# Optimization experiments

Hardware: AMD Instinct MI355X
Metric: run time of the kernel (lower is better)

Reference implementation:

```python
import jax, jax.numpy as jnp
import numpy as np

N = 100000      # nodes
E = 3200000     # edges
F_IN = 256      # in_channels
H = 64          # hidden_channels
C = 2           # out_channels
G = 128         # graphs in batch


def setup_inputs() -> dict:
    key = jax.random.key(0)
    ks = jax.random.split(key, 10)
    x = jax.random.normal(ks[0], (N, F_IN), jnp.float32)
    edge_index = jax.random.randint(ks[1], (2, E), 0, N, dtype=jnp.int64)
    batch = jnp.sort(jax.random.randint(ks[2], (N,), 0, G, dtype=jnp.int64))
    s = 0.05
    W1 = jax.random.normal(ks[3], (F_IN, H), jnp.float32) * s
    b1 = jnp.zeros((H,), jnp.float32)
    W2 = jax.random.normal(ks[4], (H, H), jnp.float32) * s
    b2 = jnp.zeros((H,), jnp.float32)
    fc_W = jax.random.normal(ks[5], (H, C), jnp.float32) * s
    fc_b = jnp.zeros((C,), jnp.float32)
    return {"x": x, "edge_index": edge_index, "batch": batch,
            "W1": W1, "b1": b1, "W2": W2, "b2": b2,
            "fc_W": fc_W, "fc_b": fc_b}


def _gcn_layer(h, src, dst, norm, W, b, n_nodes):
    # PyG GCNConv: linear transform first, then normalized aggregate, then bias
    h = h @ W                                   # [N, H]
    msg = h[src] * norm[:, None]                # [E+N, H] gather + scale
    out = jax.ops.segment_sum(msg, dst, num_segments=n_nodes)
    return out + b


def reference(x, edge_index, batch, W1, b1, W2, b2, fc_W, fc_b):
    n_nodes = x.shape[0]
    # add self loops (GCNConv default)
    loop = jnp.arange(n_nodes, dtype=edge_index.dtype)
    src = jnp.concatenate([edge_index[0], loop])
    dst = jnp.concatenate([edge_index[1], loop])
    # symmetric normalization D^{-1/2} (A+I) D^{-1/2}
    deg = jax.ops.segment_sum(jnp.ones_like(src, dtype=x.dtype), dst,
                              num_segments=n_nodes)
    deg_isqrt = jnp.where(deg > 0, jax.lax.rsqrt(deg), 0.0)
    norm = deg_isqrt[src] * deg_isqrt[dst]

    h = jax.nn.relu(_gcn_layer(x, src, dst, norm, W1, b1, n_nodes))
    h = jax.nn.relu(_gcn_layer(h, src, dst, norm, W2, b2, n_nodes))

    # global mean pool over graphs
    n_graphs = G
    sums = jax.ops.segment_sum(h, batch, num_segments=n_graphs)
    cnts = jax.ops.segment_sum(jnp.ones((n_nodes,), h.dtype), batch,
                               num_segments=n_graphs)
    pooled = sums / jnp.clip(cnts, 1.0)[:, None]  # [G, H]
    return pooled @ fc_W + fc_b                   # [G, C]
```

## Files before the change

kernel.cpp:

```cpp
#include <hip/hip_runtime.h>
#include <hip/hip_bf16.h>


#define F_IN 256
#define HDIM 64
#define BR_SHIFT 7
#define BRANGE 128
#define BCAP 4608
#define CHUNK 8192
#define NBK 788

typedef short short8 __attribute__((ext_vector_type(8)));
typedef short short4v __attribute__((ext_vector_type(4)));
typedef float float4v __attribute__((ext_vector_type(4)));
typedef _Float16 half_t;

__device__ __forceinline__ unsigned bf16_rn(float f) {
  unsigned u = __builtin_bit_cast(unsigned, f);
  return (u + 0x7FFFu + ((u >> 16) & 1u)) >> 16;
}
__device__ __forceinline__ float bf16_to_f32(unsigned h) {
  return __builtin_bit_cast(float, h << 16);
}

__global__ __launch_bounds__(256) void bin_kernel(
    const int* __restrict__ src, const int* __restrict__ dst,
    int* __restrict__ gcur, int* __restrict__ entries, int E, int nb) {
  __shared__ int out32[CHUNK];
  __shared__ int pref[NBK + 1];
  __shared__ int cur[NBK];
  __shared__ int gbase[NBK];
  __shared__ int sscan[256];
  const int tid = threadIdx.x;
  for (int i = tid; i < nb; i += 256) cur[i] = 0;
  __syncthreads();
  long e0 = (long)blockIdx.x * CHUNK;
  int cnt = (int)min((long)CHUNK, (long)E - e0);
  for (int i = tid; i < cnt; i += 256)
    atomicAdd(&cur[dst[e0 + i] >> BR_SHIFT], 1);
  __syncthreads();
  int b0 = tid * 4;
  int h[4];
  int s = 0;
#pragma unroll
  for (int i = 0; i < 4; ++i) {
    h[i] = (b0 + i < nb) ? cur[b0 + i] : 0;
    s += h[i];
  }
  int x = s;
  sscan[tid] = x;
  __syncthreads();
  for (int off = 1; off < 256; off <<= 1) {
    int t = (tid >= off) ? sscan[tid - off] : 0;
    __syncthreads();
    sscan[tid] += t;
    __syncthreads();
  }
  int run = sscan[tid] - x;
#pragma unroll
  for (int i = 0; i < 4; ++i) {
    if (b0 + i < nb) {
      pref[b0 + i] = run;
      cur[b0 + i] = run;
      if (h[i] > 0) gbase[b0 + i] = atomicAdd(&gcur[b0 + i], h[i]);
      run += h[i];
    }
  }
  if (tid == 0) pref[nb] = cnt;
  __syncthreads();
  for (int i = tid; i < cnt; i += 256) {
    int d = dst[e0 + i];
    int sv = src[e0 + i];
    int b = d >> BR_SHIFT;
    int r = atomicAdd(&cur[b], 1);
    out32[r] = ((d & (BRANGE - 1)) << 17) | sv;
  }
  __syncthreads();
  for (int j = tid; j < cnt; j += 256) {
    int lo = 0, hi = nb - 1;
    while (lo < hi) {
      int mid = (lo + hi + 1) >> 1;
      if (pref[mid] <= j) lo = mid; else hi = mid - 1;
    }
    int b = lo;
    int slot = gbase[b] + (j - pref[b]);
    if (slot < BCAP) entries[(size_t)b * BCAP + slot] = out32[j];
  }
}

__global__ __launch_bounds__(256) void bucket_scan_kernel(
    const int* __restrict__ gcur, int* __restrict__ bbase,
    int* __restrict__ rowptr, int nb, int N, int E) {
  __shared__ int sscan[256];
  const int tid = threadIdx.x;
  int b0 = tid * 4;
  int h[4];
  int s = 0;
#pragma unroll
  for (int i = 0; i < 4; ++i) {
    h[i] = (b0 + i < nb) ? min(gcur[b0 + i], BCAP) : 0;
    s += h[i];
  }
  int x = s;
  sscan[tid] = x;
  __syncthreads();
  for (int off = 1; off < 256; off <<= 1) {
    int t = (tid >= off) ? sscan[tid - off] : 0;
    __syncthreads();
    sscan[tid] += t;
    __syncthreads();
  }
  int run = sscan[tid] - x;
#pragma unroll
  for (int i = 0; i < 4; ++i) {
    if (b0 + i < nb) {
      bbase[b0 + i] = run;
      run += h[i];
    }
  }
  if (tid == 0) rowptr[N] = E;
}

__global__ __launch_bounds__(256) void csr_build_kernel(
    const int* __restrict__ entries, const int* __restrict__ gcur,
    const int* __restrict__ bbase, int* __restrict__ rowptr,
    float* __restrict__ dnorm, int* __restrict__ csr, int N) {
  __shared__ int lbuf[BCAP];
  __shared__ int lcnt[BRANGE];
  __shared__ int lpref[BRANGE];
  __shared__ int lcur[BRANGE];
  const int b = blockIdx.x, tid = threadIdx.x;
  const int v0 = b * BRANGE;
  const int nloc = min(BRANGE, N - v0);
  if (tid < BRANGE) lcnt[tid] = 0;
  __syncthreads();
  const int cnt = min(gcur[b], BCAP);
  const int base = bbase[b];
  const int* ep = entries + (size_t)b * BCAP;
  for (int i = tid; i < cnt; i += 256) atomicAdd(&lcnt[ep[i] >> 17], 1);
  __syncthreads();
  if (tid < BRANGE) lpref[tid] = lcnt[tid];
  __syncthreads();
  for (int off = 1; off < BRANGE; off <<= 1) {
    int t = 0;
    if (tid < BRANGE && tid >= off) t = lpref[tid - off];
    __syncthreads();
    if (tid < BRANGE) lpref[tid] += t;
    __syncthreads();
  }
  if (tid < BRANGE) {
    int excl = lpref[tid] - lcnt[tid];
    lcur[tid] = excl;
    if (tid < nloc) {
      rowptr[v0 + tid] = base + excl;
      dnorm[v0 + tid] = rsqrtf((float)lcnt[tid] + 1.0f);
    }
  }
  __syncthreads();
  for (int i = tid; i < cnt; i += 256) {
    int e = ep[i];
    int dl = e >> 17;
    int pos = atomicAdd(&lcur[dl], 1);
    if (pos < BCAP) lbuf[pos] = e & 0x1FFFF;
  }
  __syncthreads();
  int* outp = csr + base;
  for (int i = tid; i < cnt; i += 256) outp[i] = lbuf[i];
}

template <int K>
__global__ __launch_bounds__(256) void wfrag_kernel(
    const float* __restrict__ W, short* __restrict__ whi,
    short* __restrict__ wlo) {
  constexpr int KS = K / 32;
  int slot = blockIdx.x * 256 + threadIdx.x;
  if (slot >= 4 * KS * 64 * 8) return;
  int j = slot & 7;
  int lane = (slot >> 3) & 63;
  int fk = slot >> 9;
  int ks = fk % KS;
  int ct = fk / KS;
  int k = ks * 32 + (lane >> 4) * 8 + j;
  int n = ct * 16 + (lane & 15);
  float w = W[k * 64 + n];
  unsigned h = bf16_rn(w);
  unsigned l = bf16_rn(w - bf16_to_f32(h));
  whi[slot] = (short)h;
  wlo[slot] = (short)l;
}

template <int K, typename OT>
__global__ __launch_bounds__(512) void mfma_gemm_kernel(
    const float* __restrict__ X, const short* __restrict__ whi,
    const short* __restrict__ wlo, const float* __restrict__ dnorm,
    OT* __restrict__ out, int N) {
  constexpr int KS = K / 32;
  constexpr int P = K + 8;
  __shared__ __align__(16) short Ahi[64 * P];
  __shared__ __align__(16) short Alo[64 * P];
  const int tid = threadIdx.x;
  const long base = (long)blockIdx.x * 64;
  constexpr int C4 = K / 4;
  constexpr int NL = 64 * C4 / 512;
#pragma unroll
  for (int i = 0; i < NL; ++i) {
    int idx = tid + i * 512;
    int row = idx / C4;
    int c4 = idx % C4;
    long r = base + row;
    if (r >= N) r = N - 1;
    float4v v = *(const float4v*)&X[(size_t)r * K + c4 * 4];
    short4v hv, lv;
#pragma unroll
    for (int j = 0; j < 4; ++j) {
      float f = v[j];
      unsigned h = bf16_rn(f);
      unsigned l = bf16_rn(f - bf16_to_f32(h));
      hv[j] = (short)h;
      lv[j] = (short)l;
    }
    *(short4v*)&Ahi[row * P + c4 * 4] = hv;
    *(short4v*)&Alo[row * P + c4 * 4] = lv;
  }
  __syncthreads();
  const int lane = tid & 63;
  const int wave = tid >> 6;
  const int rt = wave & 3;
  const int chalf = wave >> 2;
  const int m = lane & 15;
  const int q = lane >> 4;
  const int arow = rt * 16 + m;
  float4v acc[2];
  acc[0] = (float4v){0.f, 0.f, 0.f, 0.f};
  acc[1] = (float4v){0.f, 0.f, 0.f, 0.f};
  for (int ks = 0; ks < KS; ++ks) {
    int koff = ks * 32 + q * 8;
    short8 ah = *(const short8*)&Ahi[arow * P + koff];
    short8 al = *(const short8*)&Alo[arow * P + koff];
#pragma unroll
    for (int cc = 0; cc < 2; ++cc) {
      int ct = chalf * 2 + cc;
      size_t fo = ((size_t)(ct * KS + ks) * 64 + lane) * 8;
      short8 bh = *(const short8*)&whi[fo];
      short8 bl = *(const short8*)&wlo[fo];
      acc[cc] = __builtin_amdgcn_mfma_f32_16x16x32_bf16(ah, bh, acc[cc], 0, 0, 0);
      acc[cc] = __builtin_amdgcn_mfma_f32_16x16x32_bf16(ah, bl, acc[cc], 0, 0, 0);
      acc[cc] = __builtin_amdgcn_mfma_f32_16x16x32_bf16(al, bh, acc[cc], 0, 0, 0);
    }
  }
#pragma unroll
  for (int reg = 0; reg < 4; ++reg) {
    long grow = base + rt * 16 + q * 4 + reg;
    if (grow < N) {
      float dn = dnorm[grow];
#pragma unroll
      for (int cc = 0; cc < 2; ++cc) {
        int ct = chalf * 2 + cc;
        out[grow * 64 + ct * 16 + m] = (OT)(acc[cc][reg] * dn);
      }
    }
  }
}

__global__ __launch_bounds__(256) void gather_agg_kernel(
    const half_t* __restrict__ hs, const int* __restrict__ rowptr,
    const int* __restrict__ csr, const float* __restrict__ dnorm,
    const float* __restrict__ bias, float* __restrict__ hout, int N) {
  const int lane = threadIdx.x & 63;
  const int wave = __builtin_amdgcn_readfirstlane((int)(threadIdx.x >> 6));
  int v = blockIdx.x * 4 + wave;
  if (v >= N) return;
  int beg = rowptr[v], end = rowptr[v + 1];
  float a0 = (float)hs[(size_t)v * 64 + lane], a1 = 0.f, a2 = 0.f, a3 = 0.f;
  int j = beg;
  for (; j + 4 <= end; j += 4) {
    int s0 = csr[j], s1 = csr[j + 1], s2 = csr[j + 2], s3 = csr[j + 3];
    a0 += (float)hs[(size_t)s0 * 64 + lane];
    a1 += (float)hs[(size_t)s1 * 64 + lane];
    a2 += (float)hs[(size_t)s2 * 64 + lane];
    a3 += (float)hs[(size_t)s3 * 64 + lane];
  }
  for (; j < end; ++j) a0 += (float)hs[(size_t)csr[j] * 64 + lane];
  float val = dnorm[v] * ((a0 + a1) + (a2 + a3)) + bias[lane];
  hout[(size_t)v * 64 + lane] = fmaxf(val, 0.f);
}

__global__ __launch_bounds__(256) void gather_agg_pool_kernel(
    const half_t* __restrict__ hs, const int* __restrict__ rowptr,
    const int* __restrict__ csr, const float* __restrict__ dnorm,
    const float* __restrict__ bias, const int* __restrict__ batch,
    float* __restrict__ pooled, int N) {
  const int lane = threadIdx.x & 63;
  const int wave = __builtin_amdgcn_readfirstlane((int)(threadIdx.x >> 6));
  int v = blockIdx.x * 4 + wave;
  if (v >= N) return;
  int beg = rowptr[v], end = rowptr[v + 1];
  float a0 = (float)hs[(size_t)v * 64 + lane], a1 = 0.f, a2 = 0.f, a3 = 0.f;
  int j = beg;
  for (; j + 4 <= end; j += 4) {
    int s0 = csr[j], s1 = csr[j + 1], s2 = csr[j + 2], s3 = csr[j + 3];
    a0 += (float)hs[(size_t)s0 * 64 + lane];
    a1 += (float)hs[(size_t)s1 * 64 + lane];
    a2 += (float)hs[(size_t)s2 * 64 + lane];
    a3 += (float)hs[(size_t)s3 * 64 + lane];
  }
  for (; j < end; ++j) a0 += (float)hs[(size_t)csr[j] * 64 + lane];
  float val = dnorm[v] * ((a0 + a1) + (a2 + a3)) + bias[lane];
  val = fmaxf(val, 0.f);
  atomicAdd(&pooled[(size_t)batch[v] * 64 + lane], val);
}

__global__ __launch_bounds__(256) void final_fc_kernel(
    const float* __restrict__ pooled, const int* __restrict__ batch,
    const float* __restrict__ fcW, const float* __restrict__ fcb,
    float* __restrict__ out, int G, int N) {
  int t = blockIdx.x * 256 + threadIdx.x;
  if (t < G * 2) {
    int g = t >> 1, c = t & 1;
    int lo = 0, hi = N;
    while (lo < hi) { int m = (lo + hi) >> 1; if (batch[m] < g) lo = m + 1; else hi = m; }
    int lb = lo;
    lo = 0; hi = N;
    while (lo < hi) { int m = (lo + hi) >> 1; if (batch[m] <= g) lo = m + 1; else hi = m; }
    int cntg = lo - lb;
    float inv = 1.0f / fmaxf((float)cntg, 1.0f);
    float acc = fcb[c];
#pragma unroll
    for (int h = 0; h < 64; ++h)
      acc = fmaf(pooled[g * 64 + h] * inv, fcW[h * 2 + c], acc);
    out[t] = acc;
  }
}

extern "C" void kernel_launch(void* const* d_in, const int* in_sizes, int n_in,
                              void* d_out, int out_size, void* d_ws, size_t ws_size,
                              hipStream_t stream) {
  const float* x   = (const float*)d_in[0];
  const int*   ei  = (const int*)d_in[1];
  const int*   bat = (const int*)d_in[2];
  const float* W1  = (const float*)d_in[3];
  const float* b1  = (const float*)d_in[4];
  const float* W2  = (const float*)d_in[5];
  const float* b2  = (const float*)d_in[6];
  const float* fcW = (const float*)d_in[7];
  const float* fcb = (const float*)d_in[8];
  float* out = (float*)d_out;

  const int N = in_sizes[0] / F_IN;
  const int E = in_sizes[1] / 2;
  const int G = out_size / 2;
  const int* src = ei;
  const int* dst = ei + E;
  const int nb  = (N + BRANGE - 1) >> BR_SHIFT;

  auto aln = [](size_t v) { return (v + 63) & ~(size_t)63; };
  char* w = (char*)d_ws;
  int*    entries = (int*)w;     w += aln((size_t)nb * BCAP * 4);
  int*    gcur    = (int*)w;     w += aln((size_t)nb * 4);
  int*    bbase   = (int*)w;     w += aln((size_t)nb * 4);
  int*    rowptr  = (int*)w;     w += aln((size_t)(N + 1) * 4);
  float*  dnorm   = (float*)w;   w += aln((size_t)N * 4);
  int*    csr     = (int*)w;     w += aln((size_t)E * 4);
  half_t* hs      = (half_t*)w;  w += aln((size_t)N * 64 * 2);
  float*  h1      = (float*)w;   w += aln((size_t)N * 64 * 4);
  float*  pooled  = (float*)w;   w += aln((size_t)G * 64 * 4);
  short*  whi1    = (short*)w;   w += aln((size_t)F_IN * 64 * 2);
  short*  wlo1    = (short*)w;   w += aln((size_t)F_IN * 64 * 2);
  short*  whi2    = (short*)w;   w += aln((size_t)HDIM * 64 * 2);
  short*  wlo2    = (short*)w;   w += aln((size_t)HDIM * 64 * 2);

  hipMemsetAsync(gcur, 0, (size_t)nb * 4, stream);
  hipMemsetAsync(pooled, 0, (size_t)G * 64 * 4, stream);

  wfrag_kernel<F_IN><<<(F_IN * 64 * 8 / 8 + 255) / 256, 256, 0, stream>>>(W1, whi1, wlo1);
  wfrag_kernel<HDIM><<<(HDIM * 64 * 8 / 8 + 255) / 256, 256, 0, stream>>>(W2, whi2, wlo2);

  bin_kernel<<<(E + CHUNK - 1) / CHUNK, 256, 0, stream>>>(
      src, dst, gcur, entries, E, nb);
  bucket_scan_kernel<<<1, 256, 0, stream>>>(gcur, bbase, rowptr, nb, N, E);
  csr_build_kernel<<<nb, 256, 0, stream>>>(entries, gcur, bbase, rowptr,
                                           dnorm, csr, N);

  mfma_gemm_kernel<F_IN, half_t><<<(N + 63) / 64, 512, 0, stream>>>(
      x, whi1, wlo1, dnorm, hs, N);
  gather_agg_kernel<<<(N + 3) / 4, 256, 0, stream>>>(hs, rowptr, csr, dnorm, b1, h1, N);

  mfma_gemm_kernel<HDIM, half_t><<<(N + 63) / 64, 512, 0, stream>>>(
      h1, whi2, wlo2, dnorm, hs, N);
  gather_agg_pool_kernel<<<(N + 3) / 4, 256, 0, stream>>>(hs, rowptr, csr, dnorm, b2, bat, pooled, N);

  final_fc_kernel<<<1, 256, 0, stream>>>(pooled, bat, fcW, fcb, out, G, N);
}
```

Measured before the change: 548.7 us.

## Split hidden features into two planar halves and gather each half separately

The GEMM now writes its fp16 output as two planes of 32 channels each instead of interleaved 64-channel rows. Each gather block handles one half for a group of nodes, with the two 32-lane halves of a wave processing alternating edges that are combined by a cross-lane shuffle. The edge loop is unrolled by 16, with eight independent accumulators. The goal is a smaller per-pass working set (a 6.4MB plane) that fits better in cache, plus more memory parallelism; the cost is twice the CSR index reads and an extra shuffle. The bin kernel's CHUNK size is also halved.

New measurement: 590.6 us. 7.6% more time.

```diff
diff --git a/kernel.cpp b/kernel.cpp
--- a/kernel.cpp
+++ b/kernel.cpp
@@ -7,7 +7,7 @@
 #define BR_SHIFT 7
 #define BRANGE 128
 #define BCAP 4608
-#define CHUNK 8192
+#define CHUNK 4096
 #define NBK 788
 
 typedef short short8 __attribute__((ext_vector_type(8)));
@@ -189,17 +189,18 @@
   wlo[slot] = (short)l;
 }
 
-template <int K, typename OT>
+template <int K>
 __global__ __launch_bounds__(512) void mfma_gemm_kernel(
     const float* __restrict__ X, const short* __restrict__ whi,
     const short* __restrict__ wlo, const float* __restrict__ dnorm,
-    OT* __restrict__ out, int N) {
+    half_t* __restrict__ out, int N) {
   constexpr int KS = K / 32;
   constexpr int P = K + 8;
   __shared__ __align__(16) short Ahi[64 * P];
   __shared__ __align__(16) short Alo[64 * P];
   const int tid = threadIdx.x;
   const long base = (long)blockIdx.x * 64;
+  const size_t hstride = (size_t)N * 32;
   constexpr int C4 = K / 4;
   constexpr int NL = 64 * C4 / 512;
 #pragma unroll
@@ -256,33 +257,79 @@
 #pragma unroll
       for (int cc = 0; cc < 2; ++cc) {
         int ct = chalf * 2 + cc;
-        out[grow * 64 + ct * 16 + m] = (OT)(acc[cc][reg] * dn);
+        out[(size_t)(ct >> 1) * hstride + grow * 32 + (ct & 1) * 16 + m] =
+            (half_t)(acc[cc][reg] * dn);
       }
     }
   }
+}
+
+__device__ __forceinline__ void gather_core(
+    const half_t* __restrict__ hsh, const int* __restrict__ csr,
+    int beg, int end, int c, bool islo, int v, float& sum) {
+  float a0 = islo ? (float)hsh[(size_t)v * 32 + c] : 0.f;
+  float a1 = 0.f, a2 = 0.f, a3 = 0.f, a4 = 0.f, a5 = 0.f, a6 = 0.f, a7 = 0.f;
+  int j = beg;
+  for (; j + 16 <= end; j += 16) {
+    int e0 = csr[j],      e1 = csr[j + 1],  e2 = csr[j + 2],  e3 = csr[j + 3];
+    int e4 = csr[j + 4],  e5 = csr[j + 5],  e6 = csr[j + 6],  e7 = csr[j + 7];
+    int e8 = csr[j + 8],  e9 = csr[j + 9],  ea = csr[j + 10], eb = csr[j + 11];
+    int ec = csr[j + 12], ed = csr[j + 13], ee = csr[j + 14], ef = csr[j + 15];
+    int p0 = islo ? e0 : e1, p1 = islo ? e2 : e3;
+    int p2 = islo ? e4 : e5, p3 = islo ? e6 : e7;
+    int p4 = islo ? e8 : e9, p5 = islo ? ea : eb;
+    int p6 = islo ? ec : ed, p7 = islo ? ee : ef;
+    a0 += (float)hsh[(size_t)p0 * 32 + c];
+    a1 += (float)hsh[(size_t)p1 * 32 + c];
+    a2 += (float)hsh[(size_t)p2 * 32 + c];
+    a3 += (float)hsh[(size_t)p3 * 32 + c];
+    a4 += (float)hsh[(size_t)p4 * 32 + c];
+    a5 += (float)hsh[(size_t)p5 * 32 + c];
+    a6 += (float)hsh[(size_t)p6 * 32 + c];
+    a7 += (float)hsh[(size_t)p7 * 32 + c];
+  }
+  for (; j + 4 <= end; j += 4) {
+    int e0 = csr[j], e1 = csr[j + 1], e2 = csr[j + 2], e3 = csr[j + 3];
+    int p0 = islo ? e0 : e1, p1 = islo ? e2 : e3;
+    a0 += (float)hsh[(size_t)p0 * 32 + c];
+    a1 += (float)hsh[(size_t)p1 * 32 + c];
+  }
+  for (; j + 2 <= end; j += 2) {
+    int e0 = csr[j], e1 = csr[j + 1];
+    int p0 = islo ? e0 : e1;
+    a0 += (float)hsh[(size_t)p0 * 32 + c];
+  }
+  if (j < end) {
+    int e0 = csr[j];
+    float val = (float)hsh[(size_t)e0 * 32 + c];
+    a0 += islo ? val : 0.f;
+  }
+  float t = ((a0 + a1) + (a2 + a3)) + ((a4 + a5) + (a6 + a7));
+  sum = t + __shfl_xor(t, 32);
 }
 
 __global__ __launch_bounds__(256) void gather_agg_kernel(
     const half_t* __restrict__ hs, const int* __restrict__ rowptr,
     const int* __restrict__ csr, const float* __restrict__ dnorm,
     const float* __restrict__ bias, float* __restrict__ hout, int N) {
+  const int b = blockIdx.x;
   const int lane = threadIdx.x & 63;
   const int wave = __builtin_amdgcn_readfirstlane((int)(threadIdx.x >> 6));
-  int v = blockIdx.x * 4 + wave;
+  const int half = (b & 7) >> 2;
+  const int o = (b >> 3) * 4 + (b & 3);
+  const int v = o * 4 + wave;
   if (v >= N) return;
+  const half_t* hsh = hs + (size_t)half * N * 32;
+  const int c = lane & 31;
+  const bool islo = lane < 32;
   int beg = rowptr[v], end = rowptr[v + 1];
-  float a0 = (float)hs[(size_t)v * 64 + lane], a1 = 0.f, a2 = 0.f, a3 = 0.f;
-  int j = beg;
-  for (; j + 4 <= end; j += 4) {
-    int s0 = csr[j], s1 = csr[j + 1], s2 = csr[j + 2], s3 = csr[j + 3];
-    a0 += (float)hs[(size_t)s0 * 64 + lane];
-    a1 += (float)hs[(size_t)s1 * 64 + lane];
-    a2 += (float)hs[(size_t)s2 * 64 + lane];
-    a3 += (float)hs[(size_t)s3 * 64 + lane];
-  }
-  for (; j < end; ++j) a0 += (float)hs[(size_t)csr[j] * 64 + lane];
-  float val = dnorm[v] * ((a0 + a1) + (a2 + a3)) + bias[lane];
-  hout[(size_t)v * 64 + lane] = fmaxf(val, 0.f);
+  float sum;
+  gather_core(hsh, csr, beg, end, c, islo, v, sum);
+  if (islo) {
+    int ch = half * 32 + c;
+    float val = dnorm[v] * sum + bias[ch];
+    hout[(size_t)v * 64 + ch] = fmaxf(val, 0.f);
+  }
 }
 
 __global__ __launch_bounds__(256) void gather_agg_pool_kernel(
@@ -290,24 +337,25 @@
     const int* __restrict__ csr, const float* __restrict__ dnorm,
     const float* __restrict__ bias, const int* __restrict__ batch,
     float* __restrict__ pooled, int N) {
+  const int b = blockIdx.x;
   const int lane = threadIdx.x & 63;
   const int wave = __builtin_amdgcn_readfirstlane((int)(threadIdx.x >> 6));
-  int v = blockIdx.x * 4 + wave;
+  const int half = (b & 7) >> 2;
+  const int o = (b >> 3) * 4 + (b & 3);
+  const int v = o * 4 + wave;
   if (v >= N) return;
+  const half_t* hsh = hs + (size_t)half * N * 32;
+  const int c = lane & 31;
+  const bool islo = lane < 32;
   int beg = rowptr[v], end = rowptr[v + 1];
-  float a0 = (float)hs[(size_t)v * 64 + lane], a1 = 0.f, a2 = 0.f, a3 = 0.f;
-  int j = beg;
-  for (; j + 4 <= end; j += 4) {
-    int s0 = csr[j], s1 = csr[j + 1], s2 = csr[j + 2], s3 = csr[j + 3];
-    a0 += (float)hs[(size_t)s0 * 64 + lane];
-    a1 += (float)hs[(size_t)s1 * 64 + lane];
-    a2 += (float)hs[(size_t)s2 * 64 + lane];
-    a3 += (float)hs[(size_t)s3 * 64 + lane];
-  }
-  for (; j < end; ++j) a0 += (float)hs[(size_t)csr[j] * 64 + lane];
-  float val = dnorm[v] * ((a0 + a1) + (a2 + a3)) + bias[lane];
-  val = fmaxf(val, 0.f);
-  atomicAdd(&pooled[(size_t)batch[v] * 64 + lane], val);
+  float sum;
+  gather_core(hsh, csr, beg, end, c, islo, v, sum);
+  if (islo) {
+    int ch = half * 32 + c;
+    float val = dnorm[v] * sum + bias[ch];
+    val = fmaxf(val, 0.f);
+    atomicAdd(&pooled[(size_t)batch[v] * 64 + ch], val);
+  }
 }
 
 __global__ __launch_bounds__(256) void final_fc_kernel(
@@ -352,6 +400,7 @@
   const int* src = ei;
   const int* dst = ei + E;
   const int nb  = (N + BRANGE - 1) >> BR_SHIFT;
+  const int ngrp = (N + 15) / 16;
 
   auto aln = [](size_t v) { return (v + 63) & ~(size_t)63; };
   char* w = (char*)d_ws;
@@ -381,13 +430,13 @@
   csr_build_kernel<<<nb, 256, 0, stream>>>(entries, gcur, bbase, rowptr,
                                            dnorm, csr, N);
 
-  mfma_gemm_kernel<F_IN, half_t><<<(N + 63) / 64, 512, 0, stream>>>(
+  mfma_gemm_kernel<F_IN><<<(N + 63) / 64, 512, 0, stream>>>(
       x, whi1, wlo1, dnorm, hs, N);
-  gather_agg_kernel<<<(N + 3) / 4, 256, 0, stream>>>(hs, rowptr, csr, dnorm, b1, h1, N);
-
-  mfma_gemm_kernel<HDIM, half_t><<<(N + 63) / 64, 512, 0, stream>>>(
+  gather_agg_kernel<<<ngrp * 8, 256, 0, stream>>>(hs, rowptr, csr, dnorm, b1, h1, N);
+
+  mfma_gemm_kernel<HDIM><<<(N + 63) / 64, 512, 0, stream>>>(
       h1, whi2, wlo2, dnorm, hs, N);
-  gather_agg_pool_kernel<<<(N + 3) / 4, 256, 0, stream>>>(hs, rowptr, csr, dnorm, b2, bat, pooled, N);
+  gather_agg_pool_kernel<<<ngrp * 8, 256, 0, stream>>>(hs, rowptr, csr, dnorm, b2, bat, pooled, N);
 
   final_fc_kernel<<<1, 256, 0, stream>>>(pooled, bat, fcW, fcb, out, G, N);
 }
```
